# Optimization experiments

Measured on AMD Instinct MI355X. Metric: run time of the kernel, lower is better.

Reference implementation:

```python
import jax, jax.numpy as jnp
import numpy as np

# Module constants derived from init_kwargs
XYZ_MIN = np.array([-40.0, -40.0, -1.0], dtype=np.float32)
XYZ_MAX = np.array([40.0, 40.0, 5.4], dtype=np.float32)
STEPSIZE = 0.5
VOX = (200, 200, 16)
NUM_VOXELS = VOX[0] * VOX[1] * VOX[2]
VOXEL_SIZE = float((np.prod(XYZ_MAX - XYZ_MIN) / NUM_VOXELS) ** (1.0 / 3.0))  # = 0.4
N_SAMPLES = int(np.linalg.norm(np.array([VOX[0] // 2, VOX[1] // 2, VOX[2] // 2]) + 1) / STEPSIZE) + 1  # 287


def setup_inputs() -> dict:
    key = jax.random.key(0)
    k1, k2, k3 = jax.random.split(key, 3)
    rays_o = jax.random.uniform(k1, (6, 90, 160, 3), dtype=jnp.float32)   # camera origins near scene center
    rays_d = jax.random.normal(k2, (6, 90, 160, 3), dtype=jnp.float32)    # ray directions
    voxel = jax.random.normal(k3, (1, 200, 200, 16), dtype=jnp.float32)   # density grid (C=1, X, Y, Z)
    return {"rays_o": rays_o, "rays_d": rays_d, "voxel": voxel}


def trilinear_sample(grid, pts):
    """align_corners=True trilinear interpolation.
    grid: (C, Dx, Dy, Dz) laid out as (world-x, world-y, world-z) axes
    pts:  (M, 3) world coords. Out-of-range pts are clamped (they are masked later).
    Returns (C, M).
    """
    xyz_min = jnp.asarray(XYZ_MIN)
    xyz_max = jnp.asarray(XYZ_MAX)
    sizes = jnp.asarray(np.array(grid.shape[1:], dtype=np.float32))
    u = (pts - xyz_min) / (xyz_max - xyz_min)              # normalized [0,1]
    idx = jnp.clip(u * (sizes - 1.0), 0.0, sizes - 1.0)    # voxel-space coords
    i0 = jnp.clip(jnp.floor(idx), 0.0, sizes - 2.0).astype(jnp.int32)
    f = idx - i0.astype(idx.dtype)                          # fractional offsets
    x0, y0, z0 = i0[:, 0], i0[:, 1], i0[:, 2]
    fx, fy, fz = f[:, 0], f[:, 1], f[:, 2]
    out = jnp.zeros((grid.shape[0], pts.shape[0]), dtype=grid.dtype)
    for dx in (0, 1):
        wx = fx if dx else (1.0 - fx)
        for dy in (0, 1):
            wy = fy if dy else (1.0 - fy)
            for dz in (0, 1):
                wz = fz if dz else (1.0 - fz)
                corner = grid[:, x0 + dx, y0 + dy, z0 + dz]   # (C, M) gather
                out = out + corner * (wx * wy * wz)[None, :]
    return out


def reference(rays_o, rays_d, voxel):
    xyz_min = jnp.asarray(XYZ_MIN)
    xyz_max = jnp.asarray(XYZ_MAX)
    ro = rays_o.reshape(-1, 3)                                # (M, 3)
    rd = rays_d.reshape(-1, 3)                                # (M, 3)
    # eval-mode sampling: deterministic Zval shared by all rays
    zval = STEPSIZE * VOXEL_SIZE * jnp.arange(N_SAMPLES, dtype=jnp.float32)  # (N,)
    pts = ro[:, None, :] + rd[:, None, :] * zval[None, :, None]             # (M, N, 3)
    mask_out = jnp.any((pts < xyz_min) | (pts > xyz_max), axis=-1)          # (M, N)
    density = trilinear_sample(voxel, pts.reshape(-1, 3))                   # (1, M*N)
    density = density.reshape(pts.shape[0], N_SAMPLES)                      # (M, N)
    # alpha compositing (render_type='density')
    delta = zval[-1] - zval[-2]                                             # constant step length
    alpha = jnp.where(mask_out, 0.0, 1.0 - jnp.exp(-jax.nn.softplus(density) * delta))
    trans = jnp.cumprod(jnp.clip(1.0 - alpha, 1e-10, None), axis=-1)        # (M, N)
    alphainv_cum = jnp.concatenate([jnp.ones_like(trans[:, :1]), trans], axis=-1)
    weights = alpha * alphainv_cum[:, :-1]                                  # (M, N)
    depth = jnp.sum(weights * zval[None, :], axis=-1)                       # (M,)
    return depth
```

## Files before the change

### kernel.cpp

```cpp
#include <hip/hip_runtime.h>
#include <math.h>

#define N_RAYS 86400
#define N_SAMP 287
#define GRP_W  16
#define N_CHUNK ((N_SAMP + GRP_W - 1) / GRP_W)
#define LOG2E 1.4426950408889634f

#define ROW_SHR_OLD1(x, N)                                                   \
    __int_as_float(__builtin_amdgcn_update_dpp(                              \
        0x3f800000 , __float_as_int(x), 0x110 | (N), 0xF, 0xF, false))

#define SWZ(x, pat) __int_as_float(__builtin_amdgcn_ds_swizzle(__float_as_int(x), (pat)))
#define SWZ_BCAST15 0x1F0
#define SWZ_XOR(m)  (((m) << 10) | 0x1F)

__global__ __launch_bounds__(256) void nerf_depth_kernel(
    const float* __restrict__ rays_o,
    const float* __restrict__ rays_d,
    const float* __restrict__ voxel,
    float* __restrict__ depth_out,
    float stepf, float delta)
{
    const int lane = threadIdx.x & 63;
    const int sub  = lane & (GRP_W - 1);
    const int grp  = lane >> 4;
    const int wave = (blockIdx.x * blockDim.x + threadIdx.x) >> 6;
    const int ray  = wave * 4 + grp;

    const float ox = rays_o[3*ray+0], oy = rays_o[3*ray+1], oz = rays_o[3*ray+2];
    const float dx = rays_d[3*ray+0], dy = rays_d[3*ray+1], dz = rays_d[3*ray+2];

    const float cx1 = 199.0f / 80.0f;                  const float cx0 = 40.0f * cx1;
    const float cz1 = 15.0f / (5.4f - (-1.0f));        const float cz0 = 1.0f * cz1;
    const float negdelta = -delta;

    float T = 1.0f;
    float depth_acc = 0.0f;
    bool  done = false;

    for (int c = 0; c < N_CHUNK; ++c) {
        const int  s     = c * GRP_W + sub;
        const bool valid = (s < N_SAMP);
        const float z  = __fmul_rn(stepf, (float)s);
        const float px = __fadd_rn(ox, __fmul_rn(dx, z));
        const float py = __fadd_rn(oy, __fmul_rn(dy, z));
        const float pz = __fadd_rn(oz, __fmul_rn(dz, z));
        const bool inside = !((fmaxf(fabsf(px), fabsf(py)) > 40.0f) |
                              (pz < -1.0f) | (pz > 5.4f));
        const bool inb = (!done) && valid && inside;

        const unsigned long long bal = __ballot(inb);
        if (((unsigned)(bal >> (grp * GRP_W)) & 0xFFFFu) == 0u) done = true;
        if (__all(done)) break;

        float alpha = 0.0f, az = 0.0f;
        if (inb) {
            float ix = fminf(fmaxf(__builtin_fmaf(px, cx1, cx0), 0.0f), 199.0f);
            float iy = fminf(fmaxf(__builtin_fmaf(py, cx1, cx0), 0.0f), 199.0f);
            float iz = fminf(fmaxf(__builtin_fmaf(pz, cz1, cz0), 0.0f), 15.0f);
            int x0 = min((int)ix, 198);
            int y0 = min((int)iy, 198);
            int z0 = min((int)iz, 14);
            float fx = ix - (float)x0;
            float fy = iy - (float)y0;
            float fz = iz - (float)z0;
            const float* ba = voxel + (y0 * 16 + z0);
            const float* bb = ba + x0 * 3200;
            const float* bc = bb + 3200;
            float c000 = bb[0],  c001 = bb[1];
            float c010 = bb[16], c011 = bb[17];
            float c100 = bc[0],  c101 = bc[1];
            float c110 = bc[16], c111 = bc[17];
            float c00 = c000 + fz * (c001 - c000);
            float c01 = c010 + fz * (c011 - c010);
            float c10 = c100 + fz * (c101 - c100);
            float c11 = c110 + fz * (c111 - c110);
            float c0  = c00 + fy * (c01 - c00);
            float c1  = c10 + fy * (c11 - c10);
            float d   = c0  + fx * (c1  - c0);
            float e2 = exp2f(d * LOG2E);
            float lg = __log2f(1.0f + e2);
            alpha = 1.0f - exp2f(negdelta * lg);
            az = alpha * z;
        }

        float g = fmaxf(1.0f - alpha, 1e-10f);

        float P = g;
        P *= ROW_SHR_OLD1(P, 1);
        P *= ROW_SHR_OLD1(P, 2);
        P *= ROW_SHR_OLD1(P, 4);
        P *= ROW_SHR_OLD1(P, 8);
        float E = ROW_SHR_OLD1(P, 1);

        depth_acc = __builtin_fmaf(az, T * E, depth_acc);
        T *= SWZ(P, SWZ_BCAST15);

        if (T < 1e-6f) done = true;
    }

    depth_acc += SWZ(depth_acc, SWZ_XOR(1));
    depth_acc += SWZ(depth_acc, SWZ_XOR(2));
    depth_acc += SWZ(depth_acc, SWZ_XOR(4));
    depth_acc += SWZ(depth_acc, SWZ_XOR(8));
    if (sub == 0) depth_out[ray] = depth_acc;
}

extern "C" void kernel_launch(void* const* d_in, const int* in_sizes, int n_in,
                              void* d_out, int out_size, void* d_ws, size_t ws_size,
                              hipStream_t stream) {
    (void)in_sizes; (void)n_in; (void)d_ws; (void)ws_size; (void)out_size;
    const float* rays_o = (const float*)d_in[0];
    const float* rays_d = (const float*)d_in[1];
    const float* voxel  = (const float*)d_in[2];
    float* out = (float*)d_out;

    float rngz  = 5.4f - (-1.0f);
    float prod  = (80.0f * 80.0f) * rngz;
    float ratio = prod / 640000.0f;
    float stepf = (float)(0.5 * pow((double)ratio, 1.0 / 3.0));
    float delta = stepf * 286.0f - stepf * 285.0f;

    const int blocks = N_RAYS / 16;
    nerf_depth_kernel<<<blocks, 256, 0, stream>>>(rays_o, rays_d, voxel, out, stepf, delta);
}
```

Before: 26.93 us.

## Pack voxel corners into float4 quads to halve gather loads

Adds a pre-pass kernel that builds, for every cell, a float4 holding the (z, z+1, y+1, y+1/z+1) neighbours, and stores it in the workspace. The depth kernel then fetches two 16-byte loads per sample instead of eight scalar gathers. This trades fewer memory instructions in the hot loop for an extra launch, a 4x larger grid (about 10 MB) written and read each call, and a larger cache footprint.

```diff
diff --git a/kernel.cpp b/kernel.cpp
--- a/kernel.cpp
+++ b/kernel.cpp
@@ -6,6 +6,8 @@
 #define GRP_W  16
 #define N_CHUNK ((N_SAMP + GRP_W - 1) / GRP_W)
 #define LOG2E 1.4426950408889634f
+#define N_CELLS (200 * 200 * 16)
+#define PLANE   (200 * 16)
 
 #define ROW_SHR_OLD1(x, N)                                                   \
     __int_as_float(__builtin_amdgcn_update_dpp(                              \
@@ -15,10 +17,30 @@
 #define SWZ_BCAST15 0x1F0
 #define SWZ_XOR(m)  (((m) << 10) | 0x1F)
 
+__global__ __launch_bounds__(256) void pack_quad_kernel(
+    const float* __restrict__ v, float4* __restrict__ q)
+{
+    int idx = blockIdx.x * blockDim.x + threadIdx.x;
+    if (idx >= N_CELLS) return;
+    int z  = idx & 15;
+    int xy = idx >> 4;
+    int y  = xy % 200;
+    float a = v[idx];
+    float b = (z < 15) ? v[idx + 1]  : a;
+    float c, d;
+    if (y < 199) {
+        c = v[idx + 16];
+        d = (z < 15) ? v[idx + 17] : c;
+    } else {
+        c = a; d = b;
+    }
+    q[idx] = make_float4(a, b, c, d);
+}
+
 __global__ __launch_bounds__(256) void nerf_depth_kernel(
     const float* __restrict__ rays_o,
     const float* __restrict__ rays_d,
-    const float* __restrict__ voxel,
+    const float4* __restrict__ quad,
     float* __restrict__ depth_out,
     float stepf, float delta)
 {
@@ -65,17 +87,13 @@
             float fx = ix - (float)x0;
             float fy = iy - (float)y0;
             float fz = iz - (float)z0;
-            const float* ba = voxel + (y0 * 16 + z0);
-            const float* bb = ba + x0 * 3200;
-            const float* bc = bb + 3200;
-            float c000 = bb[0],  c001 = bb[1];
-            float c010 = bb[16], c011 = bb[17];
-            float c100 = bc[0],  c101 = bc[1];
-            float c110 = bc[16], c111 = bc[17];
-            float c00 = c000 + fz * (c001 - c000);
-            float c01 = c010 + fz * (c011 - c010);
-            float c10 = c100 + fz * (c101 - c100);
-            float c11 = c110 + fz * (c111 - c110);
+            int cell = (x0 * 200 + y0) * 16 + z0;
+            float4 q0 = quad[cell];
+            float4 q1 = quad[cell + PLANE];
+            float c00 = q0.x + fz * (q0.y - q0.x);
+            float c01 = q0.z + fz * (q0.w - q0.z);
+            float c10 = q1.x + fz * (q1.y - q1.x);
+            float c11 = q1.z + fz * (q1.w - q1.z);
             float c0  = c00 + fy * (c01 - c00);
             float c1  = c10 + fy * (c11 - c10);
             float d   = c0  + fx * (c1  - c0);
@@ -110,11 +128,12 @@
 extern "C" void kernel_launch(void* const* d_in, const int* in_sizes, int n_in,
                               void* d_out, int out_size, void* d_ws, size_t ws_size,
                               hipStream_t stream) {
-    (void)in_sizes; (void)n_in; (void)d_ws; (void)ws_size; (void)out_size;
+    (void)in_sizes; (void)n_in; (void)ws_size; (void)out_size;
     const float* rays_o = (const float*)d_in[0];
     const float* rays_d = (const float*)d_in[1];
     const float* voxel  = (const float*)d_in[2];
     float* out = (float*)d_out;
+    float4* quad = (float4*)d_ws;
 
     float rngz  = 5.4f - (-1.0f);
     float prod  = (80.0f * 80.0f) * rngz;
@@ -122,6 +141,6 @@
     float stepf = (float)(0.5 * pow((double)ratio, 1.0 / 3.0));
     float delta = stepf * 286.0f - stepf * 285.0f;
 
-    const int blocks = N_RAYS / 16;
-    nerf_depth_kernel<<<blocks, 256, 0, stream>>>(rays_o, rays_d, voxel, out, stepf, delta);
+    pack_quad_kernel<<<(N_CELLS + 255) / 256, 256, 0, stream>>>(voxel, quad);
+    nerf_depth_kernel<<<N_RAYS / 16, 256, 0, stream>>>(rays_o, rays_d, quad, out, stepf, delta);
 }
```

Measured after the change: 36.06 us. 33.9% more time.

## Software-pipeline voxel gathers one chunk ahead and precompute ray exit chunk

Applied to the files above, without the earlier changes.

Splits each chunk into a load stage (sample position, trilinear indices, eight voxel gathers) and a compute stage, and prefetches the next chunk's gathers while the current chunk is composited. It replaces the per-chunk ballot early-exit with an analytic slab intersection that gives a per-ray chunk count, combined with the transmittance cutoff. The gathers now run unconditionally with clamped indices, so out-of-bounds lanes issue loads too, and register pressure rises because a full chunk of state is held across iterations.

```diff
diff --git a/kernel.cpp b/kernel.cpp
--- a/kernel.cpp
+++ b/kernel.cpp
@@ -4,7 +4,7 @@
 #define N_RAYS 86400
 #define N_SAMP 287
 #define GRP_W  16
-#define N_CHUNK ((N_SAMP + GRP_W - 1) / GRP_W)
+#define N_CHUNK 18
 #define LOG2E 1.4426950408889634f
 
 #define ROW_SHR_OLD1(x, N)                                                   \
@@ -14,6 +14,12 @@
 #define SWZ(x, pat) __int_as_float(__builtin_amdgcn_ds_swizzle(__float_as_int(x), (pat)))
 #define SWZ_BCAST15 0x1F0
 #define SWZ_XOR(m)  (((m) << 10) | 0x1F)
+
+struct PS {
+    float z, fx, fy, fz;
+    float v000, v001, v010, v011, v100, v101, v110, v111;
+    bool  inb;
+};
 
 __global__ __launch_bounds__(256) void nerf_depth_kernel(
     const float* __restrict__ rays_o,
@@ -35,55 +41,64 @@
     const float cz1 = 15.0f / (5.4f - (-1.0f));        const float cz0 = 1.0f * cz1;
     const float negdelta = -delta;
 
+    {
+    }
+    float invx = 1.0f / __fmul_rn(dx, stepf);
+    float invy = 1.0f / __fmul_rn(dy, stepf);
+    float invz = 1.0f / __fmul_rn(dz, stepf);
+    float tx = fmaxf((40.0f - ox) * invx, (-40.0f - ox) * invx);
+    float ty = fmaxf((40.0f - oy) * invy, (-40.0f - oy) * invy);
+    float tz = fmaxf((5.4f - oz) * invz, (-1.0f - oz) * invz);
+    float te = fminf(fminf(fminf(tx, ty), tz), 300.0f);
+    int s_stop = (int)te + 2;
+    const int nch = min(N_CHUNK, (s_stop >> 4) + 1);
+
+    auto stageA = [&](int c) -> PS {
+        PS p;
+        const int s = c * GRP_W + sub;
+        p.z = __fmul_rn(stepf, (float)s);
+        const float px = __fadd_rn(ox, __fmul_rn(dx, p.z));
+        const float py = __fadd_rn(oy, __fmul_rn(dy, p.z));
+        const float pz = __fadd_rn(oz, __fmul_rn(dz, p.z));
+        const bool inside = !((fmaxf(fabsf(px), fabsf(py)) > 40.0f) |
+                              (pz < -1.0f) | (pz > 5.4f));
+        p.inb = inside && (s < N_SAMP);
+        float ix = fminf(fmaxf(__builtin_fmaf(px, cx1, cx0), 0.0f), 199.0f);
+        float iy = fminf(fmaxf(__builtin_fmaf(py, cx1, cx0), 0.0f), 199.0f);
+        float iz = fminf(fmaxf(__builtin_fmaf(pz, cz1, cz0), 0.0f), 15.0f);
+        int x0 = min((int)ix, 198);
+        int y0 = min((int)iy, 198);
+        int z0 = min((int)iz, 14);
+        p.fx = ix - (float)x0;
+        p.fy = iy - (float)y0;
+        p.fz = iz - (float)z0;
+        const int cell = (x0 * 200 + y0) * 16 + z0;
+        p.v000 = voxel[cell];        p.v001 = voxel[cell + 1];
+        p.v010 = voxel[cell + 16];   p.v011 = voxel[cell + 17];
+        p.v100 = voxel[cell + 3200]; p.v101 = voxel[cell + 3201];
+        p.v110 = voxel[cell + 3216]; p.v111 = voxel[cell + 3217];
+        return p;
+    };
+
     float T = 1.0f;
     float depth_acc = 0.0f;
-    bool  done = false;
 
-    for (int c = 0; c < N_CHUNK; ++c) {
-        const int  s     = c * GRP_W + sub;
-        const bool valid = (s < N_SAMP);
-        const float z  = __fmul_rn(stepf, (float)s);
-        const float px = __fadd_rn(ox, __fmul_rn(dx, z));
-        const float py = __fadd_rn(oy, __fmul_rn(dy, z));
-        const float pz = __fadd_rn(oz, __fmul_rn(dz, z));
-        const bool inside = !((fmaxf(fabsf(px), fabsf(py)) > 40.0f) |
-                              (pz < -1.0f) | (pz > 5.4f));
-        const bool inb = (!done) && valid && inside;
+    PS cur = stageA(0);
+    int c = 0;
+    while (true) {
+        PS nxt = stageA(c + 1);
 
-        const unsigned long long bal = __ballot(inb);
-        if (((unsigned)(bal >> (grp * GRP_W)) & 0xFFFFu) == 0u) done = true;
-        if (__all(done)) break;
-
-        float alpha = 0.0f, az = 0.0f;
-        if (inb) {
-            float ix = fminf(fmaxf(__builtin_fmaf(px, cx1, cx0), 0.0f), 199.0f);
-            float iy = fminf(fmaxf(__builtin_fmaf(py, cx1, cx0), 0.0f), 199.0f);
-            float iz = fminf(fmaxf(__builtin_fmaf(pz, cz1, cz0), 0.0f), 15.0f);
-            int x0 = min((int)ix, 198);
-            int y0 = min((int)iy, 198);
-            int z0 = min((int)iz, 14);
-            float fx = ix - (float)x0;
-            float fy = iy - (float)y0;
-            float fz = iz - (float)z0;
-            const float* ba = voxel + (y0 * 16 + z0);
-            const float* bb = ba + x0 * 3200;
-            const float* bc = bb + 3200;
-            float c000 = bb[0],  c001 = bb[1];
-            float c010 = bb[16], c011 = bb[17];
-            float c100 = bc[0],  c101 = bc[1];
-            float c110 = bc[16], c111 = bc[17];
-            float c00 = c000 + fz * (c001 - c000);
-            float c01 = c010 + fz * (c011 - c010);
-            float c10 = c100 + fz * (c101 - c100);
-            float c11 = c110 + fz * (c111 - c110);
-            float c0  = c00 + fy * (c01 - c00);
-            float c1  = c10 + fy * (c11 - c10);
-            float d   = c0  + fx * (c1  - c0);
-            float e2 = exp2f(d * LOG2E);
-            float lg = __log2f(1.0f + e2);
-            alpha = 1.0f - exp2f(negdelta * lg);
-            az = alpha * z;
-        }
+        float c00 = cur.v000 + cur.fz * (cur.v001 - cur.v000);
+        float c01 = cur.v010 + cur.fz * (cur.v011 - cur.v010);
+        float c10 = cur.v100 + cur.fz * (cur.v101 - cur.v100);
+        float c11 = cur.v110 + cur.fz * (cur.v111 - cur.v110);
+        float c0  = c00 + cur.fy * (c01 - c00);
+        float c1  = c10 + cur.fy * (c11 - c10);
+        float d   = c0  + cur.fx * (c1  - c0);
+        float e2 = exp2f(d * LOG2E);
+        float lg = __log2f(1.0f + e2);
+        float alpha = 1.0f - exp2f(negdelta * lg);
+        alpha = cur.inb ? alpha : 0.0f;
 
         float g = fmaxf(1.0f - alpha, 1e-10f);
 
@@ -94,10 +109,13 @@
         P *= ROW_SHR_OLD1(P, 8);
         float E = ROW_SHR_OLD1(P, 1);
 
-        depth_acc = __builtin_fmaf(az, T * E, depth_acc);
+        depth_acc = __builtin_fmaf(alpha * cur.z, T * E, depth_acc);
         T *= SWZ(P, SWZ_BCAST15);
 
-        if (T < 1e-6f) done = true;
+        ++c;
+        bool done = (c >= nch) | (T < 1e-6f);
+        if (__all(done)) break;
+        cur = nxt;
     }
 
     depth_acc += SWZ(depth_acc, SWZ_XOR(1));
@@ -122,6 +140,5 @@
     float stepf = (float)(0.5 * pow((double)ratio, 1.0 / 3.0));
     float delta = stepf * 286.0f - stepf * 285.0f;
 
-    const int blocks = N_RAYS / 16;
-    nerf_depth_kernel<<<blocks, 256, 0, stream>>>(rays_o, rays_d, voxel, out, stepf, delta);
+    nerf_depth_kernel<<<N_RAYS / 16, 256, 0, stream>>>(rays_o, rays_d, voxel, out, stepf, delta);
 }
```

Result: slower. 33.75 us (+25.3%).

## Process two sample chunks per iteration with unconditional early-issued gathers

Applied to the files above, without the earlier changes.

The sampling loop is unrolled by two chunks and all eight trilinear corner loads for both chunks are issued up front, without a per-lane branch, so the memory latency of both gathers overlaps. Out-of-range samples are masked by zeroing alpha instead of skipping the load, and the early-exit check now runs once per pair. This adds loads for masked lanes and may run one chunk past where the old loop stopped, in exchange for more memory-level parallelism and less divergence.

```diff
diff --git a/kernel.cpp b/kernel.cpp
--- a/kernel.cpp
+++ b/kernel.cpp
@@ -4,7 +4,7 @@
 #define N_RAYS 86400
 #define N_SAMP 287
 #define GRP_W  16
-#define N_CHUNK ((N_SAMP + GRP_W - 1) / GRP_W)
+#define N_CHUNK 18
 #define LOG2E 1.4426950408889634f
 
 #define ROW_SHR_OLD1(x, N)                                                   \
@@ -37,67 +37,103 @@
 
     float T = 1.0f;
     float depth_acc = 0.0f;
-    bool  done = false;
 
-    for (int c = 0; c < N_CHUNK; ++c) {
-        const int  s     = c * GRP_W + sub;
-        const bool valid = (s < N_SAMP);
-        const float z  = __fmul_rn(stepf, (float)s);
-        const float px = __fadd_rn(ox, __fmul_rn(dx, z));
-        const float py = __fadd_rn(oy, __fmul_rn(dy, z));
-        const float pz = __fadd_rn(oz, __fmul_rn(dz, z));
-        const bool inside = !((fmaxf(fabsf(px), fabsf(py)) > 40.0f) |
-                              (pz < -1.0f) | (pz > 5.4f));
-        const bool inb = (!done) && valid && inside;
+    for (int c = 0; c < N_CHUNK; c += 2) {
+        const int   sA  = c * GRP_W + sub;
+        const float zA  = __fmul_rn(stepf, (float)sA);
+        const float pxA = __fadd_rn(ox, __fmul_rn(dx, zA));
+        const float pyA = __fadd_rn(oy, __fmul_rn(dy, zA));
+        const float pzA = __fadd_rn(oz, __fmul_rn(dz, zA));
+        const bool inbA = !((fmaxf(fabsf(pxA), fabsf(pyA)) > 40.0f) |
+                            (pzA < -1.0f) | (pzA > 5.4f)) && (sA < N_SAMP);
+        float ixA = fminf(fmaxf(__builtin_fmaf(pxA, cx1, cx0), 0.0f), 199.0f);
+        float iyA = fminf(fmaxf(__builtin_fmaf(pyA, cx1, cx0), 0.0f), 199.0f);
+        float izA = fminf(fmaxf(__builtin_fmaf(pzA, cz1, cz0), 0.0f), 15.0f);
+        int x0A = min((int)ixA, 198);
+        int y0A = min((int)iyA, 198);
+        int z0A = min((int)izA, 14);
+        float fxA = ixA - (float)x0A;
+        float fyA = iyA - (float)y0A;
+        float fzA = izA - (float)z0A;
+        const int cellA = (x0A * 200 + y0A) * 16 + z0A;
+        float a000 = voxel[cellA];        float a001 = voxel[cellA + 1];
+        float a010 = voxel[cellA + 16];   float a011 = voxel[cellA + 17];
+        float a100 = voxel[cellA + 3200]; float a101 = voxel[cellA + 3201];
+        float a110 = voxel[cellA + 3216]; float a111 = voxel[cellA + 3217];
 
-        const unsigned long long bal = __ballot(inb);
-        if (((unsigned)(bal >> (grp * GRP_W)) & 0xFFFFu) == 0u) done = true;
-        if (__all(done)) break;
+        const int   sB  = sA + GRP_W;
+        const float zB  = __fmul_rn(stepf, (float)sB);
+        const float pxB = __fadd_rn(ox, __fmul_rn(dx, zB));
+        const float pyB = __fadd_rn(oy, __fmul_rn(dy, zB));
+        const float pzB = __fadd_rn(oz, __fmul_rn(dz, zB));
+        const bool inbB = !((fmaxf(fabsf(pxB), fabsf(pyB)) > 40.0f) |
+                            (pzB < -1.0f) | (pzB > 5.4f)) && (sB < N_SAMP);
+        float ixB = fminf(fmaxf(__builtin_fmaf(pxB, cx1, cx0), 0.0f), 199.0f);
+        float iyB = fminf(fmaxf(__builtin_fmaf(pyB, cx1, cx0), 0.0f), 199.0f);
+        float izB = fminf(fmaxf(__builtin_fmaf(pzB, cz1, cz0), 0.0f), 15.0f);
+        int x0B = min((int)ixB, 198);
+        int y0B = min((int)iyB, 198);
+        int z0B = min((int)izB, 14);
+        float fxB = ixB - (float)x0B;
+        float fyB = iyB - (float)y0B;
+        float fzB = izB - (float)z0B;
+        const int cellB = (x0B * 200 + y0B) * 16 + z0B;
+        float b000 = voxel[cellB];        float b001 = voxel[cellB + 1];
+        float b010 = voxel[cellB + 16];   float b011 = voxel[cellB + 17];
+        float b100 = voxel[cellB + 3200]; float b101 = voxel[cellB + 3201];
+        float b110 = voxel[cellB + 3216]; float b111 = voxel[cellB + 3217];
 
-        float alpha = 0.0f, az = 0.0f;
-        if (inb) {
-            float ix = fminf(fmaxf(__builtin_fmaf(px, cx1, cx0), 0.0f), 199.0f);
-            float iy = fminf(fmaxf(__builtin_fmaf(py, cx1, cx0), 0.0f), 199.0f);
-            float iz = fminf(fmaxf(__builtin_fmaf(pz, cz1, cz0), 0.0f), 15.0f);
-            int x0 = min((int)ix, 198);
-            int y0 = min((int)iy, 198);
-            int z0 = min((int)iz, 14);
-            float fx = ix - (float)x0;
-            float fy = iy - (float)y0;
-            float fz = iz - (float)z0;
-            const float* ba = voxel + (y0 * 16 + z0);
-            const float* bb = ba + x0 * 3200;
-            const float* bc = bb + 3200;
-            float c000 = bb[0],  c001 = bb[1];
-            float c010 = bb[16], c011 = bb[17];
-            float c100 = bc[0],  c101 = bc[1];
-            float c110 = bc[16], c111 = bc[17];
-            float c00 = c000 + fz * (c001 - c000);
-            float c01 = c010 + fz * (c011 - c010);
-            float c10 = c100 + fz * (c101 - c100);
-            float c11 = c110 + fz * (c111 - c110);
-            float c0  = c00 + fy * (c01 - c00);
-            float c1  = c10 + fy * (c11 - c10);
-            float d   = c0  + fx * (c1  - c0);
+        const unsigned long long bal = __ballot(inbA);
+        const bool groupDead =
+            (((unsigned)(bal >> (grp * GRP_W)) & 0xFFFFu) == 0u) | (T < 1e-6f);
+
+        {
+            float c00 = a000 + fzA * (a001 - a000);
+            float c01 = a010 + fzA * (a011 - a010);
+            float c10 = a100 + fzA * (a101 - a100);
+            float c11 = a110 + fzA * (a111 - a110);
+            float c0  = c00 + fyA * (c01 - c00);
+            float c1  = c10 + fyA * (c11 - c10);
+            float d   = c0  + fxA * (c1  - c0);
             float e2 = exp2f(d * LOG2E);
             float lg = __log2f(1.0f + e2);
-            alpha = 1.0f - exp2f(negdelta * lg);
-            az = alpha * z;
+            float alpha = 1.0f - exp2f(negdelta * lg);
+            alpha = inbA ? alpha : 0.0f;
+            float g = fmaxf(1.0f - alpha, 1e-10f);
+            float P = g;
+            P *= ROW_SHR_OLD1(P, 1);
+            P *= ROW_SHR_OLD1(P, 2);
+            P *= ROW_SHR_OLD1(P, 4);
+            P *= ROW_SHR_OLD1(P, 8);
+            float E = ROW_SHR_OLD1(P, 1);
+            depth_acc = __builtin_fmaf(alpha * zA, T * E, depth_acc);
+            T *= SWZ(P, SWZ_BCAST15);
         }
 
-        float g = fmaxf(1.0f - alpha, 1e-10f);
+        {
+            float c00 = b000 + fzB * (b001 - b000);
+            float c01 = b010 + fzB * (b011 - b010);
+            float c10 = b100 + fzB * (b101 - b100);
+            float c11 = b110 + fzB * (b111 - b110);
+            float c0  = c00 + fyB * (c01 - c00);
+            float c1  = c10 + fyB * (c11 - c10);
+            float d   = c0  + fxB * (c1  - c0);
+            float e2 = exp2f(d * LOG2E);
+            float lg = __log2f(1.0f + e2);
+            float alpha = 1.0f - exp2f(negdelta * lg);
+            alpha = inbB ? alpha : 0.0f;
+            float g = fmaxf(1.0f - alpha, 1e-10f);
+            float P = g;
+            P *= ROW_SHR_OLD1(P, 1);
+            P *= ROW_SHR_OLD1(P, 2);
+            P *= ROW_SHR_OLD1(P, 4);
+            P *= ROW_SHR_OLD1(P, 8);
+            float E = ROW_SHR_OLD1(P, 1);
+            depth_acc = __builtin_fmaf(alpha * zB, T * E, depth_acc);
+            T *= SWZ(P, SWZ_BCAST15);
+        }
 
-        float P = g;
-        P *= ROW_SHR_OLD1(P, 1);
-        P *= ROW_SHR_OLD1(P, 2);
-        P *= ROW_SHR_OLD1(P, 4);
-        P *= ROW_SHR_OLD1(P, 8);
-        float E = ROW_SHR_OLD1(P, 1);
-
-        depth_acc = __builtin_fmaf(az, T * E, depth_acc);
-        T *= SWZ(P, SWZ_BCAST15);
-
-        if (T < 1e-6f) done = true;
+        if (__all(groupDead)) break;
     }
 
     depth_acc += SWZ(depth_acc, SWZ_XOR(1));
@@ -122,6 +158,5 @@
     float stepf = (float)(0.5 * pow((double)ratio, 1.0 / 3.0));
     float delta = stepf * 286.0f - stepf * 285.0f;
 
-    const int blocks = N_RAYS / 16;
-    nerf_depth_kernel<<<blocks, 256, 0, stream>>>(rays_o, rays_d, voxel, out, stepf, delta);
+    nerf_depth_kernel<<<N_RAYS / 16, 256, 0, stream>>>(rays_o, rays_d, voxel, out, stepf, delta);
 }
```

Result: slower. 46.08 us (+71.1%).
